# Performance work log

Measured on AMD Instinct MI355X. Metric: run time of the kernel, lower is better.

## Reference

```python
import jax, jax.numpy as jnp
import numpy as np

HIDDEN = 2048
INTER = 4096
HEADS = 32
HEAD_DIM = INTER // HEADS  # 128
STATE = 128
GROUPS = 1
CONV_K = 4
CHUNK = 256
EPS = 1e-5
CONV_DIM = INTER + 2 * GROUPS * STATE  # 4352
DT_MIN, DT_MAX = 0.0, 100.0
BATCH, SEQ = 2, 4096


def _segment_sum(x):
    """Stable segment sum: returns (..., T, T) with entry [i,j] = sum_{k=j+1..i} x[k] (-inf above diag)."""
    T = x.shape[-1]
    xx = jnp.broadcast_to(x[..., None], x.shape + (T,))
    mask_lower = jnp.tril(jnp.ones((T, T), bool), -1)
    xx = jnp.where(mask_lower, xx, 0.0)
    seg = jnp.cumsum(xx, axis=-2)
    mask_incl = jnp.tril(jnp.ones((T, T), bool), 0)
    return jnp.where(mask_incl, seg, -jnp.inf)


def setup_inputs() -> dict:
    key = jax.random.key(0)
    ks = jax.random.split(key, 8)
    std = 0.02
    return {
        "hidden_states": jax.random.normal(ks[0], (BATCH, SEQ, HIDDEN), jnp.float32),
        "in_proj_w": jax.random.normal(ks[1], (INTER + CONV_DIM + HEADS, HIDDEN), jnp.float32) * std,
        "conv_w": jax.random.normal(ks[2], (CONV_DIM, 1, CONV_K), jnp.float32) * std,
        "conv_b": jnp.zeros((CONV_DIM,), jnp.float32),
        "A_log": jnp.log(jax.random.uniform(ks[3], (HEADS,), jnp.float32, 1.0, 16.0)),
        "dt_bias": jax.random.normal(ks[4], (HEADS,), jnp.float32) * 0.1,
        "D": jnp.ones((HEADS,), jnp.float32),
        "norm_w": jnp.ones((INTER,), jnp.float32),
        "out_proj_w": jax.random.normal(ks[5], (HIDDEN, INTER), jnp.float32) * (std / np.sqrt(48.0)),
    }


def reference(hidden_states, in_proj_w, conv_w, conv_b, A_log, dt_bias, D, norm_w, out_proj_w):
    b, s, _ = hidden_states.shape
    # in_proj and split into gate / conv-input / dt
    proj = hidden_states @ in_proj_w.T
    gate, hBC, dt = jnp.split(proj, [INTER, INTER + CONV_DIM], axis=-1)

    # causal depthwise conv1d (padding k-1 left, truncate to seq_len) + SiLU
    x = jnp.transpose(hBC, (0, 2, 1))  # (b, conv_dim, s)
    x = jax.lax.conv_general_dilated(
        x, conv_w, window_strides=(1,), padding=[(CONV_K - 1, 0)],
        dimension_numbers=("NCH", "OIH", "NCH"), feature_group_count=CONV_DIM)
    x = x + conv_b[None, :, None]
    hBC = jax.nn.silu(jnp.transpose(x, (0, 2, 1)))  # (b, s, conv_dim)

    xs, B, C = jnp.split(hBC, [INTER, INTER + GROUPS * STATE], axis=-1)

    A = -jnp.exp(A_log)  # (h,)
    dt = jnp.clip(jax.nn.softplus(dt + dt_bias), DT_MIN, DT_MAX)  # (b, s, h)

    xs = xs.reshape(b, s, HEADS, HEAD_DIM)
    rep = HEADS // GROUPS
    Bm = jnp.repeat(B.reshape(b, s, GROUPS, STATE), rep, axis=2)  # (b,s,h,n)
    Cm = jnp.repeat(C.reshape(b, s, GROUPS, STATE), rep, axis=2)

    pad = (-s) % CHUNK

    def padseq(t):
        return jnp.pad(t, ((0, 0), (0, pad)) + ((0, 0),) * (t.ndim - 2))

    D_res = D[None, None, :, None] * padseq(xs)  # (b, S, h, p)
    xdt = padseq(xs * dt[..., None])
    Ad = padseq(A[None, None, :] * dt)  # (b, S, h)
    Bm, Cm = padseq(Bm), padseq(Cm)

    nc = (s + pad) // CHUNK
    xdt = xdt.reshape(b, nc, CHUNK, HEADS, HEAD_DIM)
    Ad = jnp.transpose(Ad.reshape(b, nc, CHUNK, HEADS), (0, 3, 1, 2))  # (b,h,c,l)
    Bm = Bm.reshape(b, nc, CHUNK, HEADS, STATE)
    Cm = Cm.reshape(b, nc, CHUNK, HEADS, STATE)

    A_cum = jnp.cumsum(Ad, axis=-1)  # (b,h,c,l)

    # 1) intra-chunk (diagonal block) output
    L = jnp.exp(_segment_sum(Ad))  # (b,h,c,l,l)
    G = jnp.einsum("bclhn,bcshn->bclsh", Cm, Bm)
    M = G * jnp.transpose(L, (0, 2, 3, 4, 1))
    Y_diag = jnp.einsum("bclsh,bcshp->bclhp", M, xdt)

    # 2) per-chunk final states
    decay_states = jnp.exp(A_cum[:, :, :, -1:] - A_cum)  # (b,h,c,l)
    B_decay = Bm * jnp.transpose(decay_states, (0, 2, 3, 1))[..., None]
    states = jnp.einsum("bclhn,bclhp->bchpn", B_decay, xdt)  # (b,c,h,p,n)

    # 3) inter-chunk recurrence
    states = jnp.concatenate([jnp.zeros_like(states[:, :1]), states], axis=1)  # (b,c+1,h,p,n)
    chunk_sums = jnp.pad(A_cum[:, :, :, -1], ((0, 0), (0, 0), (1, 0)))  # (b,h,c+1)
    decay_chunk = jnp.exp(_segment_sum(chunk_sums))  # (b,h,c+1,c+1)
    decay_chunk = jnp.transpose(decay_chunk, (0, 2, 3, 1))  # (b,c,z,h)
    new_states = jnp.einsum("bczh,bchpn->bzhpn", decay_chunk, states)
    states = new_states[:, :-1]  # (b,c,h,p,n) state entering each chunk

    # 4) state -> output contribution
    state_decay = jnp.exp(A_cum)  # (b,h,c,l)
    Y_off = jnp.einsum("bclhn,bchpn->bclhp", Cm, states) * jnp.transpose(state_decay, (0, 2, 3, 1))[..., None]

    y = (Y_diag + Y_off).reshape(b, nc * CHUNK, HEADS, HEAD_DIM) + D_res
    y = y[:, :s].reshape(b, s, INTER)

    # gated RMSNorm
    y = y * jax.nn.silu(gate)
    var = jnp.mean(y * y, axis=-1, keepdims=True)
    y = y * jax.lax.rsqrt(var + EPS) * norm_w

    return y @ out_proj_w.T
```

## Files before the change

kernel.cpp:

```cpp
#include <hip/hip_runtime.h>

#define SEQ     4096
#define BATCH   2
#define NROWS   8192
#define HID     2048
#define INTER_  4096
#define NHEADS  32
#define HDIM    128
#define NSTATE  128
#define CDIM    4352
#define NPROJ_  8480
#define NPAD    8704
#define NCH     16
#define CHUNK_  256

typedef __attribute__((ext_vector_type(8))) short bf16x8;
typedef __attribute__((ext_vector_type(4))) short short4v;
typedef __attribute__((ext_vector_type(4))) float f32x4;

#define AS1 __attribute__((address_space(1)))
#define AS3 __attribute__((address_space(3)))

__device__ __forceinline__ float bf2f(short s) {
  union { unsigned u; float f; } x;
  x.u = ((unsigned)(unsigned short)s) << 16;
  return x.f;
}
__device__ __forceinline__ short f2bf(float f) {
  union { float f; unsigned u; } x; x.f = f;
  unsigned r = x.u + 0x7FFFu + ((x.u >> 16) & 1u);
  return (short)(r >> 16);
}

__global__ void cvt_bf16(const float* __restrict__ in, short* __restrict__ out,
                         int n4, int nsrc4) {
  int i = blockIdx.x * 256 + threadIdx.x;
  if (i >= n4) return;
  short4v o = {0, 0, 0, 0};
  if (i < nsrc4) {
    f32x4 v = *(const f32x4*)(in + (size_t)i * 4);
    o = (short4v){ f2bf(v.x), f2bf(v.y), f2bf(v.z), f2bf(v.w) };
  }
  *(short4v*)(out + (size_t)i * 4) = o;
}

template<int MODE>
__global__ __launch_bounds__(512, 1)
void gemm256(const short* __restrict__ A, const short* __restrict__ Bw,
             int M, int N, int K, int nM,
             float* __restrict__ outF, short* __restrict__ gate,
             short* __restrict__ hbc, float* __restrict__ dtraw)
{
  __shared__ __align__(16) short lds[2][2][2][256 * 32];
  const int tid = threadIdx.x;
  const int lane = tid & 63, wave = tid >> 6;
  const int l16 = lane & 15, lhi = lane >> 4;
  const int wm = wave >> 2, wn = wave & 3;

  const int bm = blockIdx.x % nM, bn = blockIdx.x / nM;
  const size_t row0 = (size_t)bm * 256;
  const int    col0 = bn * 256;

  const short* Ab  = A + row0 * K;
  const short* Bbp = Bw + (size_t)col0 * K;

  f32x4 acc[8][4];
  #pragma unroll
  for (int m = 0; m < 8; ++m)
    #pragma unroll
    for (int n = 0; n < 4; ++n) acc[m][n] = (f32x4){0.f, 0.f, 0.f, 0.f};

  auto stage = [&](int bufq, int mat, int kh, int ko) {
    const short* gsrc = mat ? Bbp : Ab;
    short* base = &lds[bufq][mat][kh][0];
    #pragma unroll
    for (int j = 0; j < 2; ++j) {
      int u = j * 512 + tid;
      int r = u >> 2;
      int g = (u & 3) ^ ((r >> 1) & 3);
      __builtin_amdgcn_global_load_lds(
          (const AS1 unsigned*)(gsrc + (size_t)r * K + ko + kh * 32 + g * 8),
          (AS3 unsigned*)(base + (j * 512 + wave * 64) * 8), 16, 0, 0);
    }
  };
  auto readA = [&](int bufq, int kh, int mh, bf16x8* a) {
    const short* base = &lds[bufq][0][kh][0];
    #pragma unroll
    for (int f = 0; f < 4; ++f) {
      int rr = wm * 128 + mh * 64 + f * 16 + l16;
      int g = lhi ^ ((rr >> 1) & 3);
      a[f] = *(const bf16x8*)(base + rr * 32 + g * 8);
    }
  };
  auto readB = [&](int bufq, int kh, bf16x8* b) {
    const short* base = &lds[bufq][1][kh][0];
    #pragma unroll
    for (int f = 0; f < 4; ++f) {
      int rr = wn * 64 + f * 16 + l16;
      int g = lhi ^ ((rr >> 1) & 3);
      b[f] = *(const bf16x8*)(base + rr * 32 + g * 8);
    }
  };

  const int nt = K / 64;
  stage(0, 0, 0, 0); stage(0, 1, 0, 0); stage(0, 0, 1, 0); stage(0, 1, 1, 0);
  asm volatile("s_waitcnt vmcnt(4)" ::: "memory");
  __builtin_amdgcn_s_barrier();

  for (int t = 0; t < nt; ++t) {
    const int buf = t & 1, nb = buf ^ 1;
    const int kon = (t + 1) * 64;
    const bool pf = (t + 1 < nt);
    bf16x8 bfr[4];

    #pragma unroll
    for (int kh = 0; kh < 2; ++kh) {
      #pragma unroll
      for (int mh = 0; mh < 2; ++mh) {
        bf16x8 a[4];
        if (mh == 0) readB(buf, kh, bfr);
        readA(buf, kh, mh, a);
        if (pf) stage(nb, mh, kh, kon);
        __builtin_amdgcn_s_barrier();
        asm volatile("s_waitcnt lgkmcnt(0)" ::: "memory");
        __builtin_amdgcn_sched_barrier(0);
        __builtin_amdgcn_s_setprio(1);
        #pragma unroll
        for (int f = 0; f < 4; ++f)
          #pragma unroll
          for (int nf = 0; nf < 4; ++nf)
            acc[mh * 4 + f][nf] =
                __builtin_amdgcn_mfma_f32_16x16x32_bf16(a[f], bfr[nf], acc[mh * 4 + f][nf], 0, 0, 0);
        __builtin_amdgcn_s_setprio(0);
        if (mh == 1) {
          if (pf) asm volatile("s_waitcnt vmcnt(4)" ::: "memory");
          else    asm volatile("s_waitcnt vmcnt(0)" ::: "memory");
        }
        __builtin_amdgcn_s_barrier();
      }
    }
  }

  #pragma unroll
  for (int mh = 0; mh < 2; ++mh) {
    #pragma unroll
    for (int f = 0; f < 4; ++f) {
      #pragma unroll
      for (int nf = 0; nf < 4; ++nf) {
        #pragma unroll
        for (int j = 0; j < 4; ++j) {
          int gr = (int)row0 + wm * 128 + mh * 64 + f * 16 + lhi * 4 + j;
          int gc = col0 + wn * 64 + nf * 16 + l16;
          float v = acc[mh * 4 + f][nf][j];
          if (MODE == 0) {
            outF[(size_t)gr * N + gc] = v;
          } else {
            if (gc < INTER_)             gate[(size_t)gr * INTER_ + gc] = f2bf(v);
            else if (gc < INTER_ + CDIM) hbc[(size_t)gr * CDIM + (gc - INTER_)] = f2bf(v);
            else if (gc < NPROJ_)        dtraw[(size_t)gr * NHEADS + (gc - INTER_ - CDIM)] = v;
          }
        }
      }
    }
  }
}

__global__ __launch_bounds__(256)
void conv_t(const short* __restrict__ hbc, const float* __restrict__ cw,
            const float* __restrict__ cb, short* __restrict__ xsT,
            short* __restrict__ Bb, short* __restrict__ Cb, short* __restrict__ BbT)
{
  __shared__ short sOut[64][130];
  int ct = blockIdx.y;
  int cl = threadIdx.x & 127;
  int rh = threadIdx.x >> 7;
  int c = ct * 128 + cl;
  int row0 = blockIdx.x * 64;
  int s0 = row0 & (SEQ - 1);
  float w0 = cw[c * 4 + 0], w1 = cw[c * 4 + 1], w2 = cw[c * 4 + 2], w3 = cw[c * 4 + 3];
  float bias = cb[c];
  int r0 = rh * 32;
  float h0, h1, h2;
  h0 = (s0 + r0 - 3 >= 0) ? bf2f(hbc[(size_t)(row0 + r0 - 3) * CDIM + c]) : 0.f;
  h1 = (s0 + r0 - 2 >= 0) ? bf2f(hbc[(size_t)(row0 + r0 - 2) * CDIM + c]) : 0.f;
  h2 = (s0 + r0 - 1 >= 0) ? bf2f(hbc[(size_t)(row0 + r0 - 1) * CDIM + c]) : 0.f;

  for (int r = r0; r < r0 + 32; ++r) {
    float xin = bf2f(hbc[(size_t)(row0 + r) * CDIM + c]);
    float a = bias + w0 * h0 + w1 * h1 + w2 * h2 + w3 * xin;
    h0 = h1; h1 = h2; h2 = xin;
    float v = a / (1.f + expf(-a));
    short bv = f2bf(v);
    if (ct < 33) sOut[r][cl] = bv;
    if (ct == 32)      Bb[(size_t)(row0 + r) * NSTATE + cl] = bv;
    else if (ct == 33) Cb[(size_t)(row0 + r) * NSTATE + cl] = bv;
  }
  if (ct >= 33) return;
  __syncthreads();
  int p = threadIdx.x >> 1, sh = (threadIdx.x & 1) * 32;
  int b = row0 >> 12;
  size_t dst;
  short* outp;
  if (ct < 32) { outp = xsT; dst = ((size_t)(b * 32 + ct) * 128 + p) * SEQ + s0 + sh; }
  else         { outp = BbT; dst = ((size_t)b * 128 + p) * SEQ + s0 + sh; }
  #pragma unroll
  for (int g = 0; g < 8; ++g) {
    short4v o;
    o[0] = sOut[sh + g * 4 + 0][p];
    o[1] = sOut[sh + g * 4 + 1][p];
    o[2] = sOut[sh + g * 4 + 2][p];
    o[3] = sOut[sh + g * 4 + 3][p];
    *(short4v*)(outp + dst + g * 4) = o;
  }
}

__global__ void dt_proc(const float* __restrict__ dtraw, const float* __restrict__ dtb,
                        float* __restrict__ dtT, int n) {
  int i = blockIdx.x * 256 + threadIdx.x;
  if (i >= n) return;
  float x = dtraw[i] + dtb[i & (NHEADS - 1)];
  float sp = (x > 20.f) ? x : log1pf(expf(x));
  float d = fminf(fmaxf(sp, 0.f), 100.f);
  int row = i >> 5, h = i & 31;
  dtT[(size_t)h * NROWS + row] = d;
}

__global__ __launch_bounds__(256)
void ssm_state(const short* __restrict__ xsT, const short* __restrict__ BbT,
               const float* __restrict__ dtT, const float* __restrict__ Alog,
               float* __restrict__ cs, float* __restrict__ dAsum)
{
  int blk = blockIdx.x;
  int h = blk & 31, cc = (blk >> 5) & 15, b = blk >> 9;
  int tid = threadIdx.x, lane = tid & 63, wave = tid >> 6;
  int l16 = lane & 15, lhi = lane >> 4;
  int s0 = cc * CHUNK_;

  __shared__ float acum[256];
  __shared__ float sdt[256];
  { float Ah = -expf(Alog[h]);
    float d = dtT[(size_t)h * NROWS + (size_t)b * SEQ + s0 + tid];
    sdt[tid] = d; acum[tid] = Ah * d; }
  for (int off = 1; off < 256; off <<= 1) {
    __syncthreads();
    float v = (tid >= off) ? acum[tid - off] : 0.f;
    __syncthreads();
    acum[tid] += v;
  }
  __syncthreads();
  float alast = acum[255];

  const short* xbase = xsT + ((size_t)(b * 32 + h) * 128) * SEQ + s0;
  const short* bbase = BbT + ((size_t)b * 128) * SEQ + s0;

  f32x4 acc[2][8];
  #pragma unroll
  for (int m = 0; m < 2; ++m)
    #pragma unroll
    for (int n = 0; n < 8; ++n) acc[m][n] = (f32x4){0.f, 0.f, 0.f, 0.f};

  for (int lt0 = 0; lt0 < 256; lt0 += 32) {
    float fe[8];
    #pragma unroll
    for (int e = 0; e < 8; ++e) {
      int kl = lt0 + lhi * 8 + e;
      fe[e] = sdt[kl] * __expf(alast - acum[kl]);
    }
    bf16x8 af[2];
    #pragma unroll
    for (int m = 0; m < 2; ++m) {
      bf16x8 raw = *(const bf16x8*)(xbase + (size_t)(wave * 32 + m * 16 + l16) * SEQ + lt0 + lhi * 8);
      bf16x8 sc;
      #pragma unroll
      for (int e = 0; e < 8; ++e) sc[e] = f2bf(bf2f(raw[e]) * fe[e]);
      af[m] = sc;
    }
    #pragma unroll
    for (int n = 0; n < 8; ++n) {
      bf16x8 bfv = *(const bf16x8*)(bbase + (size_t)(n * 16 + l16) * SEQ + lt0 + lhi * 8);
      acc[0][n] = __builtin_amdgcn_mfma_f32_16x16x32_bf16(af[0], bfv, acc[0][n], 0, 0, 0);
      acc[1][n] = __builtin_amdgcn_mfma_f32_16x16x32_bf16(af[1], bfv, acc[1][n], 0, 0, 0);
    }
  }
  size_t base = (size_t)blk * 16384;
  #pragma unroll
  for (int m = 0; m < 2; ++m)
    #pragma unroll
    for (int n = 0; n < 8; ++n)
      #pragma unroll
      for (int j = 0; j < 4; ++j) {
        int p = wave * 32 + m * 16 + lhi * 4 + j;
        int ng = n * 16 + l16;
        cs[base + (size_t)p * NSTATE + ng] = acc[m][n][j];
      }
  if (tid == 0) dAsum[blk] = alast;
}

__global__ void ssm_scan(float* __restrict__ cs, const float* __restrict__ dAsum) {
  int idx = blockIdx.x * 256 + threadIdx.x;
  int np = idx & 16383;
  int bh = idx >> 14;
  int h = bh & 31, b = bh >> 5;
  float run = 0.f;
  #pragma unroll
  for (int c = 0; c < NCH; ++c) {
    size_t base = ((size_t)((b * NCH + c) * NHEADS + h)) * 16384 + np;
    float v = cs[base];
    cs[base] = run;
    run = run * __expf(dAsum[(b * NCH + c) * NHEADS + h]) + v;
  }
}

__global__ __launch_bounds__(256)
void ssm_y(const short* __restrict__ xsT, const short* __restrict__ Bb,
           const short* __restrict__ Cb, const float* __restrict__ dtT,
           const float* __restrict__ Alog, const float* __restrict__ Dv,
           const float* __restrict__ cs, short* __restrict__ gateY)
{
  int blk = blockIdx.y, lt = blockIdx.x;
  int h = blk & 31, cc = (blk >> 5) & 15, b = blk >> 9;
  int tid = threadIdx.x, lane = tid & 63, wave = tid >> 6;
  int l16 = lane & 15, lhi = lane >> 4;
  int s0 = cc * CHUNK_;
  size_t row0 = (size_t)b * SEQ + s0;

  __shared__ float acum[256];
  __shared__ float sdt[256];
  __shared__ __align__(16) short M_lds[64 * 264];

  { float Ah = -expf(Alog[h]);
    float d = dtT[(size_t)h * NROWS + row0 + tid];
    sdt[tid] = d; acum[tid] = Ah * d; }
  for (int off = 1; off < 256; off <<= 1) {
    __syncthreads();
    float v = (tid >= off) ? acum[tid - off] : 0.f;
    __syncthreads();
    acum[tid] += v;
  }
  __syncthreads();

  float Dh = Dv[h];

  {
    f32x4 acc1[4][4];
    #pragma unroll
    for (int m = 0; m < 4; ++m)
      #pragma unroll
      for (int n = 0; n < 4; ++n) acc1[m][n] = (f32x4){0.f, 0.f, 0.f, 0.f};
    for (int kk = 0; kk < NSTATE; kk += 32) {
      bf16x8 af[4], bv[4];
      #pragma unroll
      for (int m = 0; m < 4; ++m)
        af[m] = *(const bf16x8*)(Cb + (row0 + lt * 64 + m * 16 + l16) * NSTATE + kk + lhi * 8);
      #pragma unroll
      for (int n = 0; n < 4; ++n)
        bv[n] = *(const bf16x8*)(Bb + (row0 + wave * 64 + n * 16 + l16) * NSTATE + kk + lhi * 8);
      #pragma unroll
      for (int m = 0; m < 4; ++m)
        #pragma unroll
        for (int n = 0; n < 4; ++n)
          acc1[m][n] = __builtin_amdgcn_mfma_f32_16x16x32_bf16(af[m], bv[n], acc1[m][n], 0, 0, 0);
    }
    float as_[4]; int sg_[4];
    #pragma unroll
    for (int n = 0; n < 4; ++n) { sg_[n] = wave * 64 + n * 16 + l16; as_[n] = acum[sg_[n]]; }
    #pragma unroll
    for (int m = 0; m < 4; ++m) {
      #pragma unroll
      for (int j = 0; j < 4; ++j) {
        int ll = m * 16 + lhi * 4 + j;
        int lg = lt * 64 + ll;
        float al = acum[lg];
        float dinv = Dh / fmaxf(sdt[lg], 1e-20f);
        #pragma unroll
        for (int n = 0; n < 4; ++n) {
          float v = 0.f;
          if (sg_[n] <= lg) {
            v = acc1[m][n][j] * __expf(al - as_[n]);
            if (sg_[n] == lg) v += dinv;
          }
          M_lds[ll * 264 + wave * 64 + n * 16 + l16] = f2bf(v);
        }
      }
    }
  }
  __syncthreads();

  const short* xbase = xsT + ((size_t)(b * 32 + h) * 128) * SEQ + s0;

  f32x4 accY[4][2];
  #pragma unroll
  for (int m = 0; m < 4; ++m) { accY[m][0] = (f32x4){0,0,0,0}; accY[m][1] = (f32x4){0,0,0,0}; }
  int smax = (lt + 1) * 64;
  for (int st = 0; st < smax; st += 32) {
    float fe[8];
    #pragma unroll
    for (int e = 0; e < 8; ++e) fe[e] = sdt[st + lhi * 8 + e];
    bf16x8 bv2[2];
    #pragma unroll
    for (int n = 0; n < 2; ++n) {
      bf16x8 raw = *(const bf16x8*)(xbase + (size_t)(wave * 32 + n * 16 + l16) * SEQ + st + lhi * 8);
      bf16x8 sc;
      #pragma unroll
      for (int e = 0; e < 8; ++e) sc[e] = f2bf(bf2f(raw[e]) * fe[e]);
      bv2[n] = sc;
    }
    #pragma unroll
    for (int m = 0; m < 4; ++m) {
      bf16x8 a = *(const bf16x8*)(M_lds + (m * 16 + l16) * 264 + st + lhi * 8);
      accY[m][0] = __builtin_amdgcn_mfma_f32_16x16x32_bf16(a, bv2[0], accY[m][0], 0, 0, 0);
      accY[m][1] = __builtin_amdgcn_mfma_f32_16x16x32_bf16(a, bv2[1], accY[m][1], 0, 0, 0);
    }
  }

  f32x4 accO[4][2];
  #pragma unroll
  for (int m = 0; m < 4; ++m) { accO[m][0] = (f32x4){0,0,0,0}; accO[m][1] = (f32x4){0,0,0,0}; }
  size_t pbase = (size_t)blk * 16384;
  for (int nt = 0; nt < NSTATE; nt += 32) {
    bf16x8 bv2[2];
    #pragma unroll
    for (int n = 0; n < 2; ++n) {
      int p = wave * 32 + n * 16 + l16;
      const float* src = cs + pbase + (size_t)p * NSTATE + nt + lhi * 8;
      f32x4 v0 = *(const f32x4*)src;
      f32x4 v1 = *(const f32x4*)(src + 4);
      bf16x8 sc;
      sc[0] = f2bf(v0.x); sc[1] = f2bf(v0.y); sc[2] = f2bf(v0.z); sc[3] = f2bf(v0.w);
      sc[4] = f2bf(v1.x); sc[5] = f2bf(v1.y); sc[6] = f2bf(v1.z); sc[7] = f2bf(v1.w);
      bv2[n] = sc;
    }
    #pragma unroll
    for (int m = 0; m < 4; ++m) {
      bf16x8 a = *(const bf16x8*)(Cb + (row0 + lt * 64 + m * 16 + l16) * NSTATE + nt + lhi * 8);
      accO[m][0] = __builtin_amdgcn_mfma_f32_16x16x32_bf16(a, bv2[0], accO[m][0], 0, 0, 0);
      accO[m][1] = __builtin_amdgcn_mfma_f32_16x16x32_bf16(a, bv2[1], accO[m][1], 0, 0, 0);
    }
  }

  #pragma unroll
  for (int m = 0; m < 4; ++m) {
    #pragma unroll
    for (int j = 0; j < 4; ++j) {
      int ll = m * 16 + lhi * 4 + j;
      float e = __expf(acum[lt * 64 + ll]);
      size_t row = row0 + lt * 64 + ll;
      #pragma unroll
      for (int n = 0; n < 2; ++n) {
        int p = wave * 32 + n * 16 + l16;
        size_t adr = row * INTER_ + h * HDIM + p;
        float yv = accY[m][n][j] + e * accO[m][n][j];
        float g = bf2f(gateY[adr]);
        gateY[adr] = f2bf(yv * g / (1.f + expf(-g)));
      }
    }
  }
}

__global__ __launch_bounds__(256)
void gate_norm(short* __restrict__ ybf, const float* __restrict__ nw)
{
  int row = blockIdx.x;
  int tid = threadIdx.x;
  size_t base = (size_t)row * INTER_;
  float vals[16];
  float ss = 0.f;
  #pragma unroll
  for (int i = 0; i < 16; ++i) {
    int idx = tid + i * 256;
    float v = bf2f(ybf[base + idx]);
    vals[i] = v;
    ss += v * v;
  }
  #pragma unroll
  for (int off = 32; off > 0; off >>= 1) ss += __shfl_down(ss, off);
  __shared__ float ws4[4];
  if ((tid & 63) == 0) ws4[tid >> 6] = ss;
  __syncthreads();
  float tot = ws4[0] + ws4[1] + ws4[2] + ws4[3];
  float scale = rsqrtf(tot * (1.f / 4096.f) + 1e-5f);
  #pragma unroll
  for (int i = 0; i < 16; ++i) {
    int idx = tid + i * 256;
    ybf[base + idx] = f2bf(vals[i] * scale * nw[idx]);
  }
}

extern "C" void kernel_launch(void* const* d_in, const int* in_sizes, int n_in,
                              void* d_out, int out_size, void* d_ws, size_t ws_size,
                              hipStream_t stream)
{
  const float* Xf   = (const float*)d_in[0];
  const float* W1f  = (const float*)d_in[1];
  const float* cw   = (const float*)d_in[2];
  const float* cb   = (const float*)d_in[3];
  const float* Alog = (const float*)d_in[4];
  const float* dtb  = (const float*)d_in[5];
  const float* Dv   = (const float*)d_in[6];
  const float* nw   = (const float*)d_in[7];
  const float* W2f  = (const float*)d_in[8];
  float* outp = (float*)d_out;
  char* ws = (char*)d_ws;

  size_t off = 0;
  short* Xb  = (short*)(ws + off); off += (size_t)NROWS * HID * 2;
  short* W1b = (short*)(ws + off); off += (size_t)NPAD * HID * 2;
  short* xsT = (short*)ws;
  short* W2b = (short*)(ws + off); off += (size_t)HID * INTER_ * 2;
  short* gateY = (short*)(ws + off); off += (size_t)NROWS * INTER_ * 2;
  short* hbc  = (short*)(ws + off); off += (size_t)NROWS * CDIM * 2;
  float* dtv  = (float*)(ws + off); off += (size_t)NROWS * NHEADS * 4;
  float* dtT  = (float*)(ws + off); off += (size_t)NROWS * NHEADS * 4;
  short* Bb   = (short*)(ws + off); off += (size_t)NROWS * NSTATE * 2;
  short* Cb   = (short*)(ws + off); off += (size_t)NROWS * NSTATE * 2;
  short* BbT  = (short*)(ws + off); off += (size_t)NROWS * NSTATE * 2;
  float* dAs  = (float*)(ws + off); off += 4096;
  float* cs   = (float*)hbc;

  cvt_bf16<<<(NROWS * HID / 4 + 255) / 256, 256, 0, stream>>>(
      Xf, Xb, NROWS * HID / 4, NROWS * HID / 4);
  cvt_bf16<<<(NPAD * HID / 4 + 255) / 256, 256, 0, stream>>>(
      W1f, W1b, NPAD * HID / 4, NPROJ_ * HID / 4);
  cvt_bf16<<<(HID * INTER_ / 4 + 255) / 256, 256, 0, stream>>>(
      W2f, W2b, HID * INTER_ / 4, HID * INTER_ / 4);

  gemm256<1><<<(NROWS / 256) * (NPAD / 256), 512, 0, stream>>>(
      Xb, W1b, NROWS, NPROJ_, HID, NROWS / 256, nullptr, gateY, hbc, dtv);

  dt_proc<<<(NROWS * NHEADS) / 256, 256, 0, stream>>>(dtv, dtb, dtT, NROWS * NHEADS);
  conv_t<<<dim3(NROWS / 64, 34), 256, 0, stream>>>(hbc, cw, cb, xsT, Bb, Cb, BbT);

  ssm_state<<<BATCH * NCH * NHEADS, 256, 0, stream>>>(xsT, BbT, dtT, Alog, cs, dAs);
  ssm_scan<<<(BATCH * NHEADS * 16384) / 256, 256, 0, stream>>>(cs, dAs);
  ssm_y<<<dim3(4, BATCH * NCH * NHEADS), 256, 0, stream>>>(xsT, Bb, Cb, dtT, Alog, Dv, cs, gateY);

  gate_norm<<<NROWS, 256, 0, stream>>>(gateY, nw);

  gemm256<0><<<(NROWS / 256) * (HID / 256), 512, 0, stream>>>(
      gateY, W2b, NROWS, HID, INTER_, NROWS / 256, outp, nullptr, nullptr, nullptr);
}
```

Before: 900.7 us.

## Restructure GEMM k-loop barriers and store chunk states in bf16

The GEMM main loop now issues all prefetches for a k-half first, reads both A halves and B from LDS, and runs all 32 MFMAs in one block. This cuts the barriers per k-half from two to at most one and drops the explicit lgkmcnt wait and sched_barrier. Separately, the SSM chunk states are stored, scanned and read as bf16 instead of fp32, which halves that memory traffic. The trade-off is extra rounding in the inter-chunk recurrence, and the reordered barriers raise the risk of LDS buffer hazards.

```diff
diff --git a/kernel.cpp b/kernel.cpp
--- a/kernel.cpp
+++ b/kernel.cpp
@@ -111,31 +111,22 @@
     const int buf = t & 1, nb = buf ^ 1;
     const int kon = (t + 1) * 64;
     const bool pf = (t + 1 < nt);
-    bf16x8 bfr[4];
 
     #pragma unroll
     for (int kh = 0; kh < 2; ++kh) {
-      #pragma unroll
-      for (int mh = 0; mh < 2; ++mh) {
-        bf16x8 a[4];
-        if (mh == 0) readB(buf, kh, bfr);
-        readA(buf, kh, mh, a);
-        if (pf) stage(nb, mh, kh, kon);
-        __builtin_amdgcn_s_barrier();
-        asm volatile("s_waitcnt lgkmcnt(0)" ::: "memory");
-        __builtin_amdgcn_sched_barrier(0);
-        __builtin_amdgcn_s_setprio(1);
+      if (pf) { stage(nb, 0, kh, kon); stage(nb, 1, kh, kon); }
+      bf16x8 a[8], b[4];
+      readA(buf, kh, 0, a); readA(buf, kh, 1, a + 4); readB(buf, kh, b);
+      __builtin_amdgcn_s_setprio(1);
+      #pragma unroll
+      for (int mf = 0; mf < 8; ++mf)
         #pragma unroll
-        for (int f = 0; f < 4; ++f)
-          #pragma unroll
-          for (int nf = 0; nf < 4; ++nf)
-            acc[mh * 4 + f][nf] =
-                __builtin_amdgcn_mfma_f32_16x16x32_bf16(a[f], bfr[nf], acc[mh * 4 + f][nf], 0, 0, 0);
-        __builtin_amdgcn_s_setprio(0);
-        if (mh == 1) {
-          if (pf) asm volatile("s_waitcnt vmcnt(4)" ::: "memory");
-          else    asm volatile("s_waitcnt vmcnt(0)" ::: "memory");
-        }
+        for (int nf = 0; nf < 4; ++nf)
+          acc[mf][nf] = __builtin_amdgcn_mfma_f32_16x16x32_bf16(a[mf], b[nf], acc[mf][nf], 0, 0, 0);
+      __builtin_amdgcn_s_setprio(0);
+      if (pf || kh == 0) {
+        if (pf) asm volatile("s_waitcnt vmcnt(4)" ::: "memory");
+        else    asm volatile("s_waitcnt vmcnt(0)" ::: "memory");
         __builtin_amdgcn_s_barrier();
       }
     }
@@ -228,7 +219,7 @@
 __global__ __launch_bounds__(256)
 void ssm_state(const short* __restrict__ xsT, const short* __restrict__ BbT,
                const float* __restrict__ dtT, const float* __restrict__ Alog,
-               float* __restrict__ cs, float* __restrict__ dAsum)
+               short* __restrict__ csb, float* __restrict__ dAsum)
 {
   int blk = blockIdx.x;
   int h = blk & 31, cc = (blk >> 5) & 15, b = blk >> 9;
@@ -291,12 +282,12 @@
       for (int j = 0; j < 4; ++j) {
         int p = wave * 32 + m * 16 + lhi * 4 + j;
         int ng = n * 16 + l16;
-        cs[base + (size_t)p * NSTATE + ng] = acc[m][n][j];
+        csb[base + (size_t)p * NSTATE + ng] = f2bf(acc[m][n][j]);
       }
   if (tid == 0) dAsum[blk] = alast;
 }
 
-__global__ void ssm_scan(float* __restrict__ cs, const float* __restrict__ dAsum) {
+__global__ void ssm_scan(short* __restrict__ csb, const float* __restrict__ dAsum) {
   int idx = blockIdx.x * 256 + threadIdx.x;
   int np = idx & 16383;
   int bh = idx >> 14;
@@ -305,8 +296,8 @@
   #pragma unroll
   for (int c = 0; c < NCH; ++c) {
     size_t base = ((size_t)((b * NCH + c) * NHEADS + h)) * 16384 + np;
-    float v = cs[base];
-    cs[base] = run;
+    float v = bf2f(csb[base]);
+    csb[base] = f2bf(run);
     run = run * __expf(dAsum[(b * NCH + c) * NHEADS + h]) + v;
   }
 }
@@ -315,7 +306,7 @@
 void ssm_y(const short* __restrict__ xsT, const short* __restrict__ Bb,
            const short* __restrict__ Cb, const float* __restrict__ dtT,
            const float* __restrict__ Alog, const float* __restrict__ Dv,
-           const float* __restrict__ cs, short* __restrict__ gateY)
+           const short* __restrict__ csb, short* __restrict__ gateY)
 {
   int blk = blockIdx.y, lt = blockIdx.x;
   int h = blk & 31, cc = (blk >> 5) & 15, b = blk >> 9;
@@ -416,19 +407,13 @@
   f32x4 accO[4][2];
   #pragma unroll
   for (int m = 0; m < 4; ++m) { accO[m][0] = (f32x4){0,0,0,0}; accO[m][1] = (f32x4){0,0,0,0}; }
-  size_t pbase = (size_t)blk * 16384;
+  const short* sbase = csb + (size_t)blk * 16384;
   for (int nt = 0; nt < NSTATE; nt += 32) {
     bf16x8 bv2[2];
     #pragma unroll
     for (int n = 0; n < 2; ++n) {
       int p = wave * 32 + n * 16 + l16;
-      const float* src = cs + pbase + (size_t)p * NSTATE + nt + lhi * 8;
-      f32x4 v0 = *(const f32x4*)src;
-      f32x4 v1 = *(const f32x4*)(src + 4);
-      bf16x8 sc;
-      sc[0] = f2bf(v0.x); sc[1] = f2bf(v0.y); sc[2] = f2bf(v0.z); sc[3] = f2bf(v0.w);
-      sc[4] = f2bf(v1.x); sc[5] = f2bf(v1.y); sc[6] = f2bf(v1.z); sc[7] = f2bf(v1.w);
-      bv2[n] = sc;
+      bv2[n] = *(const bf16x8*)(sbase + (size_t)p * NSTATE + nt + lhi * 8);
     }
     #pragma unroll
     for (int m = 0; m < 4; ++m) {
@@ -515,7 +500,7 @@
   short* Cb   = (short*)(ws + off); off += (size_t)NROWS * NSTATE * 2;
   short* BbT  = (short*)(ws + off); off += (size_t)NROWS * NSTATE * 2;
   float* dAs  = (float*)(ws + off); off += 4096;
-  float* cs   = (float*)hbc;
+  short* csb  = (short*)hbc;
 
   cvt_bf16<<<(NROWS * HID / 4 + 255) / 256, 256, 0, stream>>>(
       Xf, Xb, NROWS * HID / 4, NROWS * HID / 4);
@@ -530,9 +515,9 @@
   dt_proc<<<(NROWS * NHEADS) / 256, 256, 0, stream>>>(dtv, dtb, dtT, NROWS * NHEADS);
   conv_t<<<dim3(NROWS / 64, 34), 256, 0, stream>>>(hbc, cw, cb, xsT, Bb, Cb, BbT);
 
-  ssm_state<<<BATCH * NCH * NHEADS, 256, 0, stream>>>(xsT, BbT, dtT, Alog, cs, dAs);
-  ssm_scan<<<(BATCH * NHEADS * 16384) / 256, 256, 0, stream>>>(cs, dAs);
-  ssm_y<<<dim3(4, BATCH * NCH * NHEADS), 256, 0, stream>>>(xsT, Bb, Cb, dtT, Alog, Dv, cs, gateY);
+  ssm_state<<<BATCH * NCH * NHEADS, 256, 0, stream>>>(xsT, BbT, dtT, Alog, csb, dAs);
+  ssm_scan<<<(BATCH * NHEADS * 16384) / 256, 256, 0, stream>>>(csb, dAs);
+  ssm_y<<<dim3(4, BATCH * NCH * NHEADS), 256, 0, stream>>>(xsT, Bb, Cb, dtT, Alog, Dv, csb, gateY);
 
   gate_norm<<<NROWS, 256, 0, stream>>>(gateY, nw);
 
```

Result: faster. 842.6 us (-6.5%).
